# Optimization experiments

Hardware: AMD Instinct MI355X
Metric: run time of the kernel (lower is better)

Reference implementation:

```python
import jax, jax.numpy as jnp
import numpy as np

B, S, D = 2, 2048, 2048
H, DK, DV = 16, 128, 128
K_DIM = H * DK
V_DIM = H * DV
CONV_DIM = 2 * K_DIM + V_DIM
KS = 4
EPS = 1e-6


def setup_inputs() -> dict:
    key = jax.random.key(0)
    ks = jax.random.split(key, 9)
    sc = lambda k, shape, s=0.02: jax.random.normal(k, shape, jnp.float32) * s
    return {
        "hidden_states": jax.random.normal(ks[0], (B, S, D), jnp.float32),
        "attention_mask": jnp.ones((B, S), jnp.float32),
        "W_qkv": sc(ks[1], (CONV_DIM, D)),
        "conv_w": sc(ks[2], (CONV_DIM, 1, KS), 0.2),   # depthwise kernel [C,1,K]
        "conv_b": jnp.zeros((CONV_DIM,), jnp.float32),
        "W_z": sc(ks[3], (V_DIM, D)),
        "W_b": sc(ks[4], (H, D)),
        "W_a": sc(ks[5], (H, D)),
        "dt_bias": jnp.ones((H,), jnp.float32),
        "A_log": jnp.log(jax.random.uniform(ks[6], (H,), jnp.float32, 0.5, 8.0)),
        "norm_weight": jnp.zeros((DV,), jnp.float32),
        "W_out": sc(ks[7], (D, V_DIM)),
    }


def _l2norm(x):
    return x * jax.lax.rsqrt(jnp.sum(x * x, -1, keepdims=True) + 1e-6)


def _gated_delta_rule(q, k, v, g, beta):
    # q,k: [B,S,H,DK]; v: [B,S,H,DV]; g,beta: [B,S,H]
    q = _l2norm(q) * (DK ** -0.5)
    k = _l2norm(k)

    def step(state, inp):
        # state: [B,H,DK,DV]
        qt, kt, vt, gt, bt = inp
        state = state * jnp.exp(gt)[..., None, None]          # gated decay
        kv = jnp.einsum('bhk,bhkv->bhv', kt, state)           # k^T S
        delta = (vt - kv) * bt[..., None]                     # delta-rule correction
        state = state + kt[..., :, None] * delta[..., None, :]
        ot = jnp.einsum('bhk,bhkv->bhv', qt, state)
        return state, ot

    xs = tuple(jnp.moveaxis(a, 1, 0) for a in (q, k, v, g, beta))  # time-major
    state0 = jnp.zeros((B, H, DK, DV), jnp.float32)
    _, o = jax.lax.scan(step, state0, xs)
    return jnp.moveaxis(o, 0, 1)  # [B,S,H,DV]


def reference(hidden_states, attention_mask, W_qkv, conv_w, conv_b, W_z, W_b,
              W_a, dt_bias, A_log, norm_weight, W_out):
    x = hidden_states * attention_mask[:, :, None]
    mixed = jnp.einsum('bsd,cd->bsc', x, W_qkv)               # [B,S,CONV_DIM]
    # causal depthwise conv over time
    xc = jnp.moveaxis(mixed, 1, 2)                            # [B,C,S]
    xc = jax.lax.conv_general_dilated(xc, conv_w, (1,), [(KS - 1, 0)],
                                      feature_group_count=CONV_DIM)
    xc = xc + conv_b[None, :, None]
    mixed = jax.nn.silu(jnp.moveaxis(xc, 2, 1))               # [B,S,C]
    q, k, v = jnp.split(mixed, [K_DIM, 2 * K_DIM], axis=-1)
    q = q.reshape(B, S, H, DK)
    k = k.reshape(B, S, H, DK)
    v = v.reshape(B, S, H, DV)
    z = jnp.einsum('bsd,vd->bsv', x, W_z).reshape(B, S, H, DV)
    beta = jax.nn.sigmoid(jnp.einsum('bsd,hd->bsh', x, W_b))
    g = -jnp.exp(A_log) * jax.nn.softplus(jnp.einsum('bsd,hd->bsh', x, W_a) + dt_bias)
    o = _gated_delta_rule(q, k, v, g, beta)                   # [B,S,H,DV]
    # gated RMSNorm over head_v_dim
    o = o * jax.lax.rsqrt(jnp.mean(o * o, -1, keepdims=True) + EPS)
    o = o * (1.0 + norm_weight)
    o = o * jax.nn.silu(z)
    return jnp.einsum('bsv,dv->bsd', o.reshape(B, S, V_DIM), W_out)
```

## Files before the change

### kernel.cpp

```cpp
#include <hip/hip_runtime.h>
#include <hip/hip_bf16.h>
#include <math.h>

#define BB 2
#define SS 2048
#define DD 2048
#define HH 16
#define CONVC 6144
#define MM (BB*SS)

#define CH 64
#define NCH 32
#define CD_KTS 0
#define CD_TV  16384
#define CD_TP  32768
#define CD_AQ  40960
#define CD_PV  49152
#define CD_PC  49408
#define CD_STRIDE 49664

typedef __bf16 bf16_t;
typedef __bf16 bf16x8 __attribute__((ext_vector_type(8)));
typedef __bf16 bf16x4 __attribute__((ext_vector_type(4)));
typedef float  f32x4  __attribute__((ext_vector_type(4)));

#define GLOBAL_AS __attribute__((address_space(1)))
#define LDS_AS    __attribute__((address_space(3)))

#define MFMA16(a,b,c) __builtin_amdgcn_mfma_f32_16x16x32_bf16((a),(b),(c),0,0,0)

__global__ __launch_bounds__(256) void cast_all_kernel(
    const float* __restrict__ hs, const float* __restrict__ amask,
    const float* __restrict__ Wqkv, const float* __restrict__ Wz,
    const float* __restrict__ Wb, const float* __restrict__ Wa,
    const float* __restrict__ Wout,
    bf16_t* __restrict__ x_bf, bf16_t* __restrict__ wB,
    bf16_t* __restrict__ wba, bf16_t* __restrict__ woutb)
{
  const long N0 = (long)MM*DD/4;
  const long N1 = N0 + (long)CONVC*DD/4;
  const long N2 = N1 + (long)DD*DD/4;
  const long N3 = N2 + 16*DD/4;
  const long N4 = N3 + 16*DD/4;
  const long N5 = N4 + (long)DD*DD/4;
  for (long i = (long)blockIdx.x*256 + threadIdx.x; i < N5; i += (long)gridDim.x*256) {
    const float* src; bf16_t* dst; float m = 1.f;
    if (i < N0)      { long j=i;    src = hs   + j*4; dst = x_bf + j*4; m = amask[(j*4)/DD]; }
    else if (i < N1) { long j=i-N0; src = Wqkv + j*4; dst = wB + j*4; }
    else if (i < N2) { long j=i-N1; src = Wz   + j*4; dst = wB + (size_t)CONVC*DD + j*4; }
    else if (i < N3) { long j=i-N2; src = Wb   + j*4; dst = wba + j*4; }
    else if (i < N4) { long j=i-N3; src = Wa   + j*4; dst = wba + 16*DD + j*4; }
    else             { long j=i-N4; src = Wout + j*4; dst = woutb + j*4; }
    float4 v = *(const float4*)src;
    bf16x4 o4;
    o4[0]=(bf16_t)(v.x*m); o4[1]=(bf16_t)(v.y*m);
    o4[2]=(bf16_t)(v.z*m); o4[3]=(bf16_t)(v.w*m);
    *(bf16x4*)dst = o4;
  }
}

__global__ __launch_bounds__(64) void betag3_kernel(
    const bf16_t* __restrict__ xbf, const bf16_t* __restrict__ wba,
    const float* __restrict__ dtb, const float* __restrict__ Alog,
    float2* __restrict__ gb_t)
{
  const int blk = blockIdx.x;
  const int lane = threadIdx.x;
  const int fr = lane & 15, fq = lane >> 4;
  const long tok0 = (long)blk*16;

  f32x4 acc0 = {0,0,0,0}, acc1 = {0,0,0,0};
  const bf16_t* ar = xbf + (tok0 + fr)*DD + fq*8;
  const bf16_t* b0 = wba + fr*DD + fq*8;
  const bf16_t* b1 = wba + (16+fr)*DD + fq*8;
  #pragma unroll 4
  for (int ks=0; ks<64; ++ks) {
    bf16x8 a8 = *(const bf16x8*)(ar + ks*32);
    bf16x8 p8 = *(const bf16x8*)(b0 + ks*32);
    bf16x8 q8 = *(const bf16x8*)(b1 + ks*32);
    acc0 = MFMA16(a8, p8, acc0);
    acc1 = MFMA16(a8, q8, acc1);
  }
  const int h = fr;
  float eA = expf(Alog[h]);
  float db = dtb[h];
  #pragma unroll
  for (int r=0;r<4;r++) {
    long tok = tok0 + fq*4 + r;
    int b = (int)(tok >> 11), s = (int)(tok & (SS-1));
    float beta = 1.f/(1.f+expf(-acc0[r]));
    float tt2 = acc1[r] + db;
    float sp = (tt2 > 20.f) ? tt2 : log1pf(expf(tt2));
    float g  = -eA * sp;
    gb_t[((long)b*HH + h)*SS + s] = make_float2(g, beta);
  }
}

__global__ __launch_bounds__(512) void gemm_fused(
    const bf16_t* __restrict__ A, const bf16_t* __restrict__ Bm,
    bf16_t* __restrict__ Cmix, bf16_t* __restrict__ Cz, int K, int nbn)
{
  extern __shared__ char gsm[];
  const int t    = threadIdx.x;
  const int lane = t & 63;
  const int wid  = t >> 6;
  const int wm   = wid >> 2, wn = wid & 3;
  const int fr   = lane & 15, fq = lane >> 4;

  const int nwg = gridDim.x;
  const int wg  = ((int)blockIdx.x & 7)*(nwg >> 3) + ((int)blockIdx.x >> 3);
  const int grp = wg / (nbn*4);
  const int rem = wg - grp*(nbn*4);
  const long bm = grp*4 + (rem & 3);
  const long bn = rem >> 2;

  int rowS[2], colS[2];
  #pragma unroll
  for (int i=0;i<2;i++) {
    int L  = (i*512 + t)*16;
    int Ls = L ^ (((L>>9)&1)<<5);
    rowS[i] = (Ls>>10)*16 + ((Ls&1023)>>6);
    colS[i] = (Ls&63)>>1;
  }
  const bf16_t* Ab = A  + (bm*256)*(long)K;
  const bf16_t* Bb = Bm + (bn*256)*(long)K;

  f32x4 acc[8][4];
  #pragma unroll
  for (int i=0;i<8;i++)
    #pragma unroll
    for (int j=0;j<4;j++) acc[i][j] = (f32x4){0.f,0.f,0.f,0.f};

  const int aoff = fr*64 + ((fq*16) ^ ((fr&8)<<2));

  auto stage = [&](int buf, int oper, int kh, int kt) {
    const bf16_t* srcb = oper ? Bb : Ab;
    char* dst0 = gsm + oper*65536 + buf*32768 + kh*16384 + t*16;
    #pragma unroll
    for (int i=0;i<2;i++) {
      const bf16_t* src = srcb + (long)rowS[i]*K + kt*64 + kh*32 + colS[i];
      __builtin_amdgcn_global_load_lds((const GLOBAL_AS void*)src,
          (LDS_AS void*)(dst0 + i*8192), 16, 0, 0);
    }
  };

  stage(0,0,0,0); stage(0,1,0,0); stage(0,0,1,0); stage(0,1,1,0);
  asm volatile("s_waitcnt vmcnt(4)" ::: "memory");
  __builtin_amdgcn_s_barrier();

  bf16x8 bfr[4];
  int cb = 0;
  const int KT = K >> 6;
  for (int kt=0; kt<KT; ++kt) {
    const int ktn = (kt+1 < KT) ? kt+1 : kt;
    const char* abuf = gsm + cb*32768;
    const char* bbuf = gsm + 65536 + cb*32768;

    #pragma unroll
    for (int ph=0; ph<4; ph++) {
      const int kh = ph >> 1, mh = ph & 1;
      bf16x8 af[4];
      #pragma unroll
      for (int j=0;j<4;j++)
        af[j] = *(const bf16x8*)(abuf + kh*16384 + (wm*8 + mh*4 + j)*1024 + aoff);
      if (mh == 0) {
        #pragma unroll
        for (int n=0;n<4;n++)
          bfr[n] = *(const bf16x8*)(bbuf + kh*16384 + (wn*4+n)*1024 + aoff);
      }
      stage(cb^1, mh, kh, ktn);
      if (mh == 1) {
        __builtin_amdgcn_sched_barrier(0);
        asm volatile("s_waitcnt vmcnt(4)" ::: "memory");
      }
      __builtin_amdgcn_sched_barrier(0);
      __builtin_amdgcn_s_barrier();
      asm volatile("s_waitcnt lgkmcnt(0)" ::: "memory");
      __builtin_amdgcn_sched_barrier(0);
      __builtin_amdgcn_s_setprio(1);
      #pragma unroll
      for (int j=0;j<4;j++)
        #pragma unroll
        for (int n=0;n<4;n++)
          acc[mh*4+j][n] = MFMA16(af[j], bfr[n], acc[mh*4+j][n]);
      __builtin_amdgcn_s_setprio(0);
    }
    cb ^= 1;
  }
  __syncthreads();

  bf16_t* Co;
  long No, colb;
  if (bn < 24) { Co = Cmix; No = CONVC; colb = bn*256; }
  else         { Co = Cz;   No = DD;    colb = (bn-24)*256; }

  #pragma unroll
  for (int mi=0;mi<8;mi++) {
    #pragma unroll
    for (int ni=0;ni<4;ni++) {
      long row = bm*256 + wm*128 + mi*16 + fq*4;
      long col = colb + wn*64 + ni*16 + fr;
      #pragma unroll
      for (int r=0;r<4;r++)
        Co[(row+r)*No + col] = (bf16_t)acc[mi][ni][r];
    }
  }
}

template<bool OUT_BF16>
__global__ __launch_bounds__(512) void gemm256(
    const bf16_t* __restrict__ A, const bf16_t* __restrict__ Bm,
    void* __restrict__ Cp, int M, int N, int K, int nbn)
{
  extern __shared__ char gsm[];
  const int t    = threadIdx.x;
  const int lane = t & 63;
  const int wid  = t >> 6;
  const int wm   = wid >> 2, wn = wid & 3;
  const int fr   = lane & 15, fq = lane >> 4;

  const int nwg = gridDim.x;
  const int wg  = ((int)blockIdx.x & 7)*(nwg >> 3) + ((int)blockIdx.x >> 3);
  const int grp = wg / (nbn*4);
  const int rem = wg - grp*(nbn*4);
  const long bm = grp*4 + (rem & 3);
  const long bn = rem >> 2;

  int rowS[2], colS[2];
  #pragma unroll
  for (int i=0;i<2;i++) {
    int L  = (i*512 + t)*16;
    int Ls = L ^ (((L>>9)&1)<<5);
    rowS[i] = (Ls>>10)*16 + ((Ls&1023)>>6);
    colS[i] = (Ls&63)>>1;
  }
  const bf16_t* Ab = A  + (bm*256)*(long)K;
  const bf16_t* Bb = Bm + (bn*128)*(long)K;

  f32x4 acc[8][2];
  #pragma unroll
  for (int i=0;i<8;i++) { acc[i][0] = (f32x4){0,0,0,0}; acc[i][1] = (f32x4){0,0,0,0}; }

  const int aoff = fr*64 + ((fq*16) ^ ((fr&8)<<2));

  auto stageA = [&](int buf, int kh, int kt) {
    char* dst0 = gsm + buf*32768 + kh*16384 + t*16;
    #pragma unroll
    for (int i=0;i<2;i++) {
      const bf16_t* src = Ab + (long)rowS[i]*K + kt*64 + kh*32 + colS[i];
      __builtin_amdgcn_global_load_lds((const GLOBAL_AS void*)src,
          (LDS_AS void*)(dst0 + i*8192), 16, 0, 0);
    }
  };
  auto stageB = [&](int buf, int kh, int kt) {
    char* dst = gsm + 65536 + buf*16384 + kh*8192 + t*16;
    const bf16_t* src = Bb + (long)rowS[0]*K + kt*64 + kh*32 + colS[0];
    __builtin_amdgcn_global_load_lds((const GLOBAL_AS void*)src,
        (LDS_AS void*)dst, 16, 0, 0);
  };

  stageA(0,0,0); stageB(0,0,0); stageA(0,1,0); stageB(0,1,0);
  asm volatile("s_waitcnt vmcnt(3)" ::: "memory");
  __builtin_amdgcn_s_barrier();

  int cb = 0;
  const int KT = K >> 6;
  for (int kt=0; kt<KT; ++kt) {
    const int ktn = (kt+1 < KT) ? kt+1 : kt;
    const char* abuf = gsm + cb*32768;
    const char* bbuf = gsm + 65536 + cb*16384;

    #pragma unroll
    for (int kh=0; kh<2; kh++) {
      bf16x8 af[8], bfr[2];
      #pragma unroll
      for (int j=0;j<8;j++)
        af[j] = *(const bf16x8*)(abuf + kh*16384 + (wm*8+j)*1024 + aoff);
      #pragma unroll
      for (int n=0;n<2;n++)
        bfr[n] = *(const bf16x8*)(bbuf + kh*8192 + (wn*2+n)*1024 + aoff);
      stageA(cb^1, kh, ktn);
      stageB(cb^1, kh, ktn);
      asm volatile("s_waitcnt vmcnt(3)" ::: "memory");
      __builtin_amdgcn_sched_barrier(0);
      __builtin_amdgcn_s_barrier();
      asm volatile("s_waitcnt lgkmcnt(0)" ::: "memory");
      __builtin_amdgcn_sched_barrier(0);
      __builtin_amdgcn_s_setprio(1);
      #pragma unroll
      for (int j=0;j<8;j++)
        #pragma unroll
        for (int n=0;n<2;n++)
          acc[j][n] = MFMA16(af[j], bfr[n], acc[j][n]);
      __builtin_amdgcn_s_setprio(0);
    }
    cb ^= 1;
  }
  __syncthreads();

  #pragma unroll
  for (int mi=0;mi<8;mi++) {
    #pragma unroll
    for (int ni=0;ni<2;ni++) {
      long row = bm*256 + wm*128 + mi*16 + fq*4;
      long col = bn*128 + wn*32 + ni*16 + fr;
      #pragma unroll
      for (int r=0;r<4;r++) {
        float v = acc[mi][ni][r];
        if (OUT_BF16) ((bf16_t*)Cp)[(row+r)*(long)N + col] = (bf16_t)v;
        else          ((float*)Cp)[(row+r)*(long)N + col] = v;
      }
    }
  }
}

__global__ __launch_bounds__(256) void conv_norm_kernel(
    const bf16_t* __restrict__ mixed, const float* __restrict__ cw,
    const float* __restrict__ cb, bf16_t* __restrict__ q_t,
    bf16_t* __restrict__ k_t, bf16_t* __restrict__ v_t)
{
  __shared__ bf16_t lx[35*392];
  __shared__ float4 lcw[384];
  __shared__ float  lcb[384];
  const int blk = blockIdx.x;
  const int st = blk & 63;
  const int h  = (blk >> 6) & 15;
  const int b  = blk >> 10;
  const int t  = threadIdx.x;
  const int s0 = st*32;

  for (int i = t; i < 384; i += 256) {
    int seg = i >> 7, d = i & 127;
    int gch = seg*2048 + h*128 + d;
    lcw[i] = ((const float4*)cw)[gch];
    lcb[i] = cb[gch];
  }
  for (int idx = t; idx < 1680; idx += 256) {
    int chunk = idx >> 4, e = idx & 15;
    int row = chunk / 3, seg = chunk - row*3;
    int s2 = s0 - 3 + row;
    bf16x8 v8;
    if (s2 >= 0) {
      v8 = *(const bf16x8*)(mixed + ((long)b*SS + s2)*CONVC + seg*2048 + h*128 + e*8);
    } else {
      #pragma unroll
      for (int j=0;j<8;j++) v8[j] = (bf16_t)0.f;
    }
    *(bf16x8*)&lx[row*392 + seg*128 + e*8] = v8;
  }
  __syncthreads();

  const int s_local = t >> 3, dg = t & 7;
  const int s  = s0 + s_local;
  const int d0 = dg*16;
  const long obase = ((long)(b*HH + h)*SS + s)*128 + d0;

  float scl_q = 0.f, scl_k = 0.f;

  #pragma unroll
  for (int seg=0; seg<3; ++seg) {
    bf16x8 xr[4][2];
    #pragma unroll
    for (int tp=0; tp<4; ++tp) {
      const bf16_t* p = &lx[(s_local + tp)*392 + seg*128 + d0];
      xr[tp][0] = *(const bf16x8*)p;
      xr[tp][1] = *(const bf16x8*)(p + 8);
    }
    float a[16];
    #pragma unroll
    for (int half=0; half<2; ++half) {
      #pragma unroll
      for (int j=0;j<8;j++) {
        int ch = seg*128 + d0 + half*8 + j;
        float4 wj = lcw[ch];
        float v = lcb[ch]
                + (float)xr[0][half][j]*wj.x + (float)xr[1][half][j]*wj.y
                + (float)xr[2][half][j]*wj.z + (float)xr[3][half][j]*wj.w;
        a[half*8+j] = v * (1.f/(1.f+expf(-v)));
      }
    }
    if (seg < 2) {
      float ss = 0.f;
      #pragma unroll
      for (int j=0;j<16;j++) ss += a[j]*a[j];
      ss += __shfl_xor(ss, 1);
      ss += __shfl_xor(ss, 2);
      ss += __shfl_xor(ss, 4);
      float scl = rsqrtf(ss + 1e-6f);
      if (seg == 0) scl_q = scl * 0.08838834764831845f;
      else          scl_k = scl;
    }
    {
      bf16_t* outp = (seg==0) ? (q_t + obase) : (seg==1) ? (k_t + obase) : (v_t + obase);
      float scl = (seg==0) ? scl_q : (seg==1) ? scl_k : 1.f;
      bf16x8 o0, o1;
      #pragma unroll
      for (int j=0;j<8;j++) { o0[j] = (bf16_t)(a[j]*scl); o1[j] = (bf16_t)(a[8+j]*scl); }
      *(bf16x8*)outp = o0;
      *(bf16x8*)(outp + 8) = o1;
    }
  }
}

__global__ __launch_bounds__(256) void chunkA_kernel(
    const bf16_t* __restrict__ q_t, const bf16_t* __restrict__ k_t,
    const bf16_t* __restrict__ v_t, const float2* __restrict__ gb_t,
    char* __restrict__ cdata)
{
  extern __shared__ char smem[];
  bf16_t* lK  = (bf16_t*)(smem);
  bf16_t* lQV = (bf16_t*)(smem + 17408);
  float*  lLf = (float*)(smem + 35840);
  float*  lXf = (float*)(smem + 52480);
  float*  gcv = (float*)(smem + 69120);
  float*  pvv = (float*)(smem + 69376);
  float*  bvv = (float*)(smem + 69632);
  float*  evv = (float*)(smem + 69888);
  float*  lP  = (float*)(smem + 70144);

  const int cd = blockIdx.x;
  const int bh = cd >> 5, c = cd & 31;
  const int t = threadIdx.x;
  const int lane = t & 63, w = t >> 6;
  const int fr = lane & 15, fq = lane >> 4;

  const bf16_t* kg = k_t + ((long)bh*SS + c*CH)*128;
  const bf16_t* qg = q_t + ((long)bh*SS + c*CH)*128;
  const bf16_t* vg = v_t + ((long)bh*SS + c*CH)*128;
  char* cdp = cdata + (long)cd*CD_STRIDE;

  #pragma unroll
  for (int ib=0; ib<4; ib++) {
    int e0 = (t + 256*ib)*8;
    int r = e0 >> 7, cc = e0 & 127;
    *(bf16x8*)&lK[r*136+cc]  = *(const bf16x8*)(kg + e0);
    *(bf16x8*)&lQV[r*136+cc] = *(const bf16x8*)(qg + e0);
  }
  if (t < 64) {
    float2 gb = gb_t[(long)bh*SS + c*CH + t];
    gcv[t] = gb.x;
    bvv[t] = gb.y;
  }
  __syncthreads();
  if (t < 64) {
    float g = gcv[t];
    #pragma unroll
    for (int off=1; off<64; off<<=1) {
      float n = __shfl_up(g, off);
      if (lane >= off) g += n;
    }
    gcv[t] = g;
  }
  __syncthreads();
  if (t < 64) {
    pvv[t] = expf(gcv[t]);
    evv[t] = expf(gcv[63] - gcv[t]);
  }

  {
    f32x4 accG[4], accQ[4];
    #pragma unroll
    for (int tn=0;tn<4;tn++){ accG[tn]=(f32x4){0,0,0,0}; accQ[tn]=(f32x4){0,0,0,0}; }
    #pragma unroll
    for (int ks=0;ks<4;ks++) {
      bf16x8 aK = *(const bf16x8*)&lK[(w*16+fr)*136 + fq*8 + ks*32];
      bf16x8 aQ = *(const bf16x8*)&lQV[(w*16+fr)*136 + fq*8 + ks*32];
      #pragma unroll
      for (int tn=0;tn<4;tn++) {
        bf16x8 bK = *(const bf16x8*)&lK[(tn*16+fr)*136 + fq*8 + ks*32];
        accG[tn] = MFMA16(aK, bK, accG[tn]);
        accQ[tn] = MFMA16(aQ, bK, accQ[tn]);
      }
    }
    bf16_t* aqg = (bf16_t*)(cdp + CD_AQ);
    #pragma unroll
    for (int tn=0;tn<4;tn++) {
      #pragma unroll
      for (int r=0;r<4;r++) {
        int tt = w*16 + fq*4 + r;
        int ii = tn*16 + fr;
        float er = expf(gcv[tt] - gcv[ii]);
        lLf[tt*65 + ii] = (ii < tt) ? bvv[tt]*er*accG[tn][r] : 0.f;
        aqg[tt*64 + ii] = (bf16_t)((ii <= tt) ? er*accQ[tn][r] : 0.f);
      }
    }
  }

  {
    const int a = w;
    float* Ub = lXf + (a*16)*65 + a*16;
    const float* Lb = lLf + (a*16)*65 + a*16;
    if (lane < 16) Ub[lane] = (lane == 0) ? 1.f : 0.f;
    for (int bb = a+1; bb < 4; bb++)
      for (int e = lane; e < 256; e += 64)
        lXf[(a*16 + (e>>4))*65 + bb*16 + (e&15)] = 0.f;
    if (lane < 16) {
      const int cc = lane;
      for (int i=1; i<16; i++) {
        float s = 0.f;
        for (int j=0; j<i; j++) s += Lb[i*65+j] * Ub[j*65+cc];
        Ub[i*65+cc] = ((i==cc)?1.f:0.f) - s;
      }
    }
  }
  __syncthreads();

  bf16_t* lVT = lQV;
  {
    const int m = t & 15;
    #pragma unroll
    for (int ib=0; ib<4; ib++) {
      int e0 = (t + 256*ib)*8;
      int r = e0 >> 7, cc = e0 & 127;
      bf16x8 v8 = *(const bf16x8*)(vg + e0);
      #pragma unroll
      for (int e=0;e<8;e++) {
        int ee = (e + m) & 7;
        lVT[(cc+ee)*72 + r] = v8[ee];
      }
    }
  }

  {
    const int i = t >> 4, j = t & 15;
    #pragma unroll
    for (int bb=0; bb<3; bb++) {
      float s = 0.f;
      const float* Mrow = lLf + ((bb+1)*16 + i)*65 + bb*16;
      const float* Ucol = lXf + (bb*16)*65 + bb*16 + j;
      #pragma unroll
      for (int k=0;k<16;k++) s += Mrow[k] * Ucol[k*65];
      lP[bb*272 + i*17 + j] = s;
    }
  }
  __syncthreads();
  {
    const int i = t >> 4, j = t & 15;
    #pragma unroll
    for (int bb=0; bb<3; bb++) {
      float s = 0.f;
      const float* Urow = lXf + ((bb+1)*16 + i)*65 + (bb+1)*16;
      const float* Pcol = lP + bb*272 + j;
      #pragma unroll
      for (int k=0;k<16;k++) s += Urow[k] * Pcol[k*17];
      lXf[((bb+1)*16 + i)*65 + bb*16 + j] = -s;
    }
  }
  __syncthreads();
  {
    const int i = t >> 4, j = t & 15;
    #pragma unroll
    for (int bb=0; bb<2; bb++) {
      float s = 0.f;
      const float* M0 = lLf + ((bb+2)*16 + i)*65 + bb*16;
      const float* U0 = lXf + (bb*16)*65 + bb*16 + j;
      const float* M1 = lLf + ((bb+2)*16 + i)*65 + (bb+1)*16;
      const float* T1 = lXf + ((bb+1)*16)*65 + bb*16 + j;
      #pragma unroll
      for (int k=0;k<16;k++) s += M0[k]*U0[k*65] + M1[k]*T1[k*65];
      lP[bb*272 + i*17 + j] = s;
    }
  }
  __syncthreads();
  {
    const int i = t >> 4, j = t & 15;
    #pragma unroll
    for (int bb=0; bb<2; bb++) {
      float s = 0.f;
      const float* Urow = lXf + ((bb+2)*16 + i)*65 + (bb+2)*16;
      const float* Pcol = lP + bb*272 + j;
      #pragma unroll
      for (int k=0;k<16;k++) s += Urow[k] * Pcol[k*17];
      lXf[((bb+2)*16 + i)*65 + bb*16 + j] = -s;
    }
  }
  __syncthreads();
  {
    const int i = t >> 4, j = t & 15;
    float s = 0.f;
    const float* M0 = lLf + (48 + i)*65 + 0;
    const float* U0 = lXf + 0*65 + j;
    const float* M1 = lLf + (48 + i)*65 + 16;
    const float* T1 = lXf + 16*65 + j;
    const float* M2 = lLf + (48 + i)*65 + 32;
    const float* T2 = lXf + 32*65 + j;
    #pragma unroll
    for (int k=0;k<16;k++) s += M0[k]*U0[k*65] + M1[k]*T1[k*65] + M2[k]*T2[k*65];
    lP[i*17 + j] = s;
  }
  __syncthreads();
  {
    const int i = t >> 4, j = t & 15;
    float s = 0.f;
    const float* Urow = lXf + (48 + i)*65 + 48;
    const float* Pcol = lP + j;
    #pragma unroll
    for (int k=0;k<16;k++) s += Urow[k] * Pcol[k*17];
    lXf[(48 + i)*65 + j] = -s;
  }
  __syncthreads();

  bf16_t* lXb = (bf16_t*)lLf;
  {
    bf16_t* tpg = (bf16_t*)(cdp + CD_TP);
    #pragma unroll
    for (int ib=0; ib<16; ib++) {
      int idx = t + ib*256; int r = idx>>6, cc = idx&63;
      float xv = lXf[r*65+cc] * bvv[cc];
      tpg[r*64+cc] = (bf16_t)(xv * pvv[cc]);
      lXb[r*72+cc] = (bf16_t)xv;
    }
  }
  __syncthreads();

  {
    f32x4 acc[8];
    #pragma unroll
    for (int tn=0;tn<8;tn++) acc[tn]=(f32x4){0,0,0,0};
    #pragma unroll
    for (int ks=0;ks<2;ks++) {
      bf16x8 aX = *(const bf16x8*)&lXb[(w*16+fr)*72 + fq*8 + ks*32];
      #pragma unroll
      for (int tn=0;tn<8;tn++) {
        bf16x8 bV = *(const bf16x8*)&lVT[(tn*16+fr)*72 + fq*8 + ks*32];
        acc[tn] = MFMA16(aX, bV, acc[tn]);
      }
    }
    bf16_t* tvg = (bf16_t*)(cdp + CD_TV);
    #pragma unroll
    for (int tn=0;tn<8;tn++)
      #pragma unroll
      for (int r=0;r<4;r++) {
        int tt = w*16 + fq*4 + r, dv = tn*16 + fr;
        tvg[tt*128 + dv] = (bf16_t)acc[tn][r];
      }
  }

  {
    bf16_t* ktg = (bf16_t*)(cdp + CD_KTS);
    int dk = t >> 1, c0 = (t & 1)*32;
    bf16_t tmp[32];
    #pragma unroll
    for (int i2=0;i2<32;i2++) {
      int i = c0 + i2;
      tmp[i2] = (bf16_t)((float)lK[i*136 + dk] * evv[i]);
    }
    #pragma unroll
    for (int s8=0;s8<4;s8++)
      *(bf16x8*)&ktg[dk*64 + c0 + s8*8] = *(bf16x8*)&tmp[s8*8];
  }
  if (t < 64) ((float*)(cdp + CD_PV))[t] = pvv[t];
  if (t == 0) *((float*)(cdp + CD_PC)) = expf(gcv[63]);
}

__global__ __launch_bounds__(256) void chunkS_kernel(
    const bf16_t* __restrict__ q_t, const bf16_t* __restrict__ k_t,
    const char* __restrict__ cdata, bf16_t* __restrict__ gD,
    bf16_t* __restrict__ gXq)
{
  extern __shared__ char smem[];
  float*  lS  = (float*)(smem);
  bf16_t* lSb = (bf16_t*)(smem + 8320);
  bf16_t* lK  = (bf16_t*)(smem + 12672);
  bf16_t* lQ  = (bf16_t*)(smem + 30080);
  bf16_t* lTp = (bf16_t*)(smem + 47488);
  bf16_t* lKT = (bf16_t*)(smem + 56704);
  bf16_t* lXT = (bf16_t*)(smem + 75136);
  bf16_t* lDT = (bf16_t*)(smem + 77952);

  const int bid = blockIdx.x;
  const int lb  = (bid & 7)*32 + (bid >> 3);
  const int bh = lb >> 3, sp = lb & 7;
  const int dv0 = sp*16;
  const int t = threadIdx.x, lane = t & 63, w = t >> 6;
  const int fr = lane & 15, fq = lane >> 4;

  #pragma unroll
  for (int ib=0; ib<8; ib++) {
    int idx = t + ib*256; int r = idx>>7, cc = idx&127;
    lS[r*129+cc] = 0.f;
    lSb[r*136+cc] = (bf16_t)0.f;
  }

  const bf16_t* kg = k_t + (long)bh*SS*128;
  const bf16_t* qg = q_t + (long)bh*SS*128;

  bf16x8 kr0,kr1,kr2,kr3, qr0,qr1,qr2,qr3, kt0,kt1,kt2,kt3, tp0,tp1;

#define STAGE_LOAD(CSRC)                                                       \
  {                                                                            \
    const char* cdl = cdata + (long)(bh*NCH + (CSRC))*CD_STRIDE;               \
    const bf16_t* kl = kg + (long)(CSRC)*CH*128;                               \
    const bf16_t* ql = qg + (long)(CSRC)*CH*128;                               \
    const bf16_t* ktl = (const bf16_t*)(cdl + CD_KTS);                         \
    const bf16_t* tpl = (const bf16_t*)(cdl + CD_TP);                          \
    int e0 = t*8, e1 = (t+256)*8, e2 = (t+512)*8, e3 = (t+768)*8;              \
    kr0 = *(const bf16x8*)(kl + e0); kr1 = *(const bf16x8*)(kl + e1);          \
    kr2 = *(const bf16x8*)(kl + e2); kr3 = *(const bf16x8*)(kl + e3);          \
    qr0 = *(const bf16x8*)(ql + e0); qr1 = *(const bf16x8*)(ql + e1);          \
    qr2 = *(const bf16x8*)(ql + e2); qr3 = *(const bf16x8*)(ql + e3);          \
    kt0 = *(const bf16x8*)(ktl + e0); kt1 = *(const bf16x8*)(ktl + e1);        \
    kt2 = *(const bf16x8*)(ktl + e2); kt3 = *(const bf16x8*)(ktl + e3);        \
    tp0 = *(const bf16x8*)(tpl + e0); tp1 = *(const bf16x8*)(tpl + e1);        \
  }

#define STAGE_WRITE()                                                          \
  {                                                                            \
    int e0 = t*8, e1 = (t+256)*8, e2 = (t+512)*8, e3 = (t+768)*8;              \
    *(bf16x8*)&lK[(e0>>7)*136 + (e0&127)] = kr0;                               \
    *(bf16x8*)&lK[(e1>>7)*136 + (e1&127)] = kr1;                               \
    *(bf16x8*)&lK[(e2>>7)*136 + (e2&127)] = kr2;                               \
    *(bf16x8*)&lK[(e3>>7)*136 + (e3&127)] = kr3;                               \
    *(bf16x8*)&lQ[(e0>>7)*136 + (e0&127)] = qr0;                               \
    *(bf16x8*)&lQ[(e1>>7)*136 + (e1&127)] = qr1;                               \
    *(bf16x8*)&lQ[(e2>>7)*136 + (e2&127)] = qr2;                               \
    *(bf16x8*)&lQ[(e3>>7)*136 + (e3&127)] = qr3;                               \
    *(bf16x8*)&lKT[(e0>>6)*72 + (e0&63)] = kt0;                                \
    *(bf16x8*)&lKT[(e1>>6)*72 + (e1&63)] = kt1;                                \
    *(bf16x8*)&lKT[(e2>>6)*72 + (e2&63)] = kt2;                                \
    *(bf16x8*)&lKT[(e3>>6)*72 + (e3&63)] = kt3;                                \
    *(bf16x8*)&lTp[(e0>>6)*72 + (e0&63)] = tp0;                                \
    *(bf16x8*)&lTp[(e1>>6)*72 + (e1&63)] = tp1;                                \
  }

  STAGE_LOAD(0);
  STAGE_WRITE();
  __syncthreads();

  for (int c=0; c<NCH; c++) {
    const int cd = bh*NCH + c;
    const char* cdp = cdata + (long)cd*CD_STRIDE;

    float tvq0, tvq1, tvq2, tvq3, pc;
    {
      const bf16_t* tvp = (const bf16_t*)(cdp + CD_TV);
      tvq0 = (float)tvp[(w*16+fq*4+0)*128 + dv0 + fr];
      tvq1 = (float)tvp[(w*16+fq*4+1)*128 + dv0 + fr];
      tvq2 = (float)tvp[(w*16+fq*4+2)*128 + dv0 + fr];
      tvq3 = (float)tvp[(w*16+fq*4+3)*128 + dv0 + fr];
      pc = *(const float*)(cdp + CD_PC);
    }
    const int cn = (c+1 < NCH) ? c+1 : c;
    STAGE_LOAD(cn);

    f32x4 aX = {0,0,0,0}, aXq = {0,0,0,0};
    #pragma unroll
    for (int ks=0; ks<4; ks++) {
      bf16x8 bS = *(const bf16x8*)&lSb[fr*136 + fq*8 + ks*32];
      bf16x8 aK = *(const bf16x8*)&lK[(w*16+fr)*136 + fq*8 + ks*32];
      bf16x8 aQ = *(const bf16x8*)&lQ[(w*16+fr)*136 + fq*8 + ks*32];
      aX  = MFMA16(aK, bS, aX);
      aXq = MFMA16(aQ, bS, aXq);
    }
    #pragma unroll
    for (int r=0;r<4;r++)
      lXT[fr*88 + (w*16+fq*4+r)] = (bf16_t)aX[r];
    __syncthreads();

    {
      f32x4 aD = {0,0,0,0};
      #pragma unroll
      for (int ks=0; ks<2; ks++) {
        bf16x8 aT = *(const bf16x8*)&lTp[(w*16+fr)*72 + fq*8 + ks*32];
        bf16x8 bX = *(const bf16x8*)&lXT[fr*88 + fq*8 + ks*32];
        aD = MFMA16(aT, bX, aD);
      }
      lDT[fr*88 + (w*16+fq*4+0)] = (bf16_t)(tvq0 - aD[0]);
      lDT[fr*88 + (w*16+fq*4+1)] = (bf16_t)(tvq1 - aD[1]);
      lDT[fr*88 + (w*16+fq*4+2)] = (bf16_t)(tvq2 - aD[2]);
      lDT[fr*88 + (w*16+fq*4+3)] = (bf16_t)(tvq3 - aD[3]);
    }
    #pragma unroll
    for (int ib=0; ib<8; ib++) {
      int idx = t + ib*256; int r = idx>>7, cc = idx&127;
      lS[r*129+cc] *= pc;
    }
    __syncthreads();

    {
      f32x4 aS0 = {0,0,0,0}, aS1 = {0,0,0,0};
      #pragma unroll
      for (int ks=0; ks<2; ks++) {
        bf16x8 aDd = *(const bf16x8*)&lDT[fr*88 + fq*8 + ks*32];
        bf16x8 bK0 = *(const bf16x8*)&lKT[(w*32+fr)*72 + fq*8 + ks*32];
        bf16x8 bK1 = *(const bf16x8*)&lKT[(w*32+16+fr)*72 + fq*8 + ks*32];
        aS0 = MFMA16(aDd, bK0, aS0);
        aS1 = MFMA16(aDd, bK1, aS1);
      }
      #pragma unroll
      for (int r=0;r<4;r++) {
        lS[(fq*4+r)*129 + w*32 + fr]      += aS0[r];
        lS[(fq*4+r)*129 + w*32 + 16 + fr] += aS1[r];
      }
    }
    #pragma unroll
    for (int r=0;r<4;r++)
      gXq[((long)cd*CH + w*16+fq*4+r)*128 + dv0 + fr] = (bf16_t)aXq[r];
    {
      int dvl = t >> 4, off = (t & 15)*4;
      *(bf16x4*)(gD + ((long)cd*128 + dv0 + dvl)*64 + off) =
          *(const bf16x4*)&lDT[dvl*88 + off];
    }
    __syncthreads();

    STAGE_WRITE();
    #pragma unroll
    for (int ib=0; ib<8; ib++) {
      int idx = t + ib*256; int r = idx>>7, cc = idx&127;
      lSb[r*136+cc] = (bf16_t)lS[r*129+cc];
    }
    __syncthreads();
  }
#undef STAGE_LOAD
#undef STAGE_WRITE
}

__global__ __launch_bounds__(256) void chunkO_kernel(
    const char* __restrict__ cdata, const bf16_t* __restrict__ gD,
    const bf16_t* __restrict__ gXq, const bf16_t* __restrict__ zfull,
    const float* __restrict__ nw, bf16_t* __restrict__ og)
{
  const int cd = blockIdx.x;
  const int bh = cd >> 5, c = cd & 31;
  const int b = bh >> 4, h = bh & 15;
  const int t = threadIdx.x, lane = t & 63, w = t >> 6;
  const int fr = lane & 15, fq = lane >> 4;

  const char* cdp = cdata + (long)cd*CD_STRIDE;
  const bf16_t* aqp = (const bf16_t*)(cdp + CD_AQ);
  const bf16_t* dp  = gD + (long)cd*128*64;
  const float*  pvp = (const float*)(cdp + CD_PV);

  f32x4 acc[8];
  #pragma unroll
  for (int tn=0;tn<8;tn++) acc[tn]=(f32x4){0,0,0,0};
  #pragma unroll
  for (int ks=0;ks<2;ks++) {
    bf16x8 aA = *(const bf16x8*)(aqp + (w*16+fr)*64 + fq*8 + ks*32);
    #pragma unroll
    for (int tn=0;tn<8;tn++) {
      bf16x8 bD = *(const bf16x8*)(dp + (tn*16+fr)*64 + fq*8 + ks*32);
      acc[tn] = MFMA16(aA, bD, acc[tn]);
    }
  }

  float ov[8][4];
  float ssum[4] = {0.f, 0.f, 0.f, 0.f};
  #pragma unroll
  for (int tn=0;tn<8;tn++)
    #pragma unroll
    for (int r=0;r<4;r++) {
      int tt = w*16+fq*4+r, dv = tn*16+fr;
      float v = pvp[tt]*(float)gXq[((long)cd*CH + tt)*128 + dv] + acc[tn][r];
      ov[tn][r] = v;
      ssum[r] += v*v;
    }
  #pragma unroll
  for (int r=0;r<4;r++) {
    ssum[r] += __shfl_xor(ssum[r], 1);
    ssum[r] += __shfl_xor(ssum[r], 2);
    ssum[r] += __shfl_xor(ssum[r], 4);
    ssum[r] += __shfl_xor(ssum[r], 8);
  }
  float rr[4];
  #pragma unroll
  for (int r=0;r<4;r++) rr[r] = rsqrtf(ssum[r]*(1.f/128.f) + 1e-6f);

  #pragma unroll
  for (int tn=0;tn<8;tn++) {
    #pragma unroll
    for (int r=0;r<4;r++) {
      int tt = w*16+fq*4+r, dv = tn*16+fr;
      long tok = (long)b*SS + c*CH + tt;
      float zn = (float)zfull[tok*DD + h*128 + dv];
      float val = ov[tn][r] * rr[r] * (1.f + nw[dv]) * (zn * (1.f/(1.f+expf(-zn))));
      og[(tok*HH + h)*128 + dv] = (bf16_t)val;
    }
  }
}

extern "C" void kernel_launch(void* const* d_in, const int* in_sizes, int n_in,
                              void* d_out, int out_size, void* d_ws, size_t ws_size,
                              hipStream_t stream)
{
  const float* hs    = (const float*)d_in[0];
  const float* amask = (const float*)d_in[1];
  const float* Wqkv  = (const float*)d_in[2];
  const float* convw = (const float*)d_in[3];
  const float* convb = (const float*)d_in[4];
  const float* Wz    = (const float*)d_in[5];
  const float* Wb    = (const float*)d_in[6];
  const float* Wa    = (const float*)d_in[7];
  const float* dtb   = (const float*)d_in[8];
  const float* Alog  = (const float*)d_in[9];
  const float* nw    = (const float*)d_in[10];
  const float* Wout  = (const float*)d_in[11];

  const size_t MB = 1024*1024;
  char* p = (char*)d_ws;
  auto alloc = [&](size_t bytes) { char* r = p; p += (bytes + 255) & ~(size_t)255; return r; };
  bf16_t* x_bf   = (bf16_t*)alloc(16*MB);
  char*   bigreg = alloc(84*MB);
  bf16_t* wba    = (bf16_t*)alloc(256*1024);
  bf16_t* woutb  = (bf16_t*)alloc(8*MB);
  bf16_t* zbuf   = (bf16_t*)alloc(16*MB);
  bf16_t* q_t    = (bf16_t*)alloc(16*MB);
  bf16_t* k_t    = (bf16_t*)alloc(16*MB);
  bf16_t* v_t    = (bf16_t*)alloc(16*MB);
  float2* gb_t   = (float2*)alloc((size_t)BB*HH*SS*8);
  size_t need = (size_t)(p - (char*)d_ws);
  if (ws_size < need) return;

  bf16_t* wB      = (bf16_t*)bigreg;
  bf16_t* mixed   = (bf16_t*)(bigreg + 34*MB);
  char*   cdata   = bigreg;
  bf16_t* gD      = x_bf;
  bf16_t* gXq     = v_t;
  bf16_t* og      = q_t;

  cast_all_kernel<<<2048, 256, 0, stream>>>(hs, amask, Wqkv, Wz, Wb, Wa, Wout,
                                            x_bf, wB, wba, woutb);

  betag3_kernel<<<MM/16, 64, 0, stream>>>(x_bf, wba, dtb, Alog, gb_t);

  gemm_fused<<<512, 512, 131072, stream>>>(x_bf, wB, mixed, zbuf, DD, 32);

  conv_norm_kernel<<<BB*HH*(SS/32), 256, 0, stream>>>(mixed, convw, convb, q_t, k_t, v_t);

  chunkA_kernel<<<BB*HH*NCH, 256, 73408, stream>>>(q_t, k_t, v_t, gb_t, cdata);
  chunkS_kernel<<<BB*HH*8, 256, 80768, stream>>>(q_t, k_t, cdata, gD, gXq);
  chunkO_kernel<<<BB*HH*NCH, 256, 0, stream>>>(cdata, gD, gXq, zbuf, nw, og);

  gemm256<false><<<256, 512, 98304, stream>>>(og, woutb, d_out, MM, DD, DD, 16);
}
```

Measured before the change: 380.3 us.

## Fuse intra-chunk output into chunkS and split out RMSNorm gating kernel

Moves the per-chunk output computation (Aq times delta plus decayed inter-chunk term) into the sequential chunkS kernel using its on-chip delta tile, so it no longer writes gD and gXq to global memory. A new lightweight per-(token,head) kernel then applies the gated RMSNorm, because each chunkS block only holds 16 value columns and cannot reduce over all 128. This removes intermediate global traffic and the chunkO kernel, but adds MFMA and LDS work (plus about 9KB more shared memory) to the latency-critical sequential kernel, and adds a small-block norm launch with 65536 blocks.

```diff
diff --git a/kernel.cpp b/kernel.cpp
--- a/kernel.cpp
+++ b/kernel.cpp
@@ -655,8 +655,7 @@
 
 __global__ __launch_bounds__(256) void chunkS_kernel(
     const bf16_t* __restrict__ q_t, const bf16_t* __restrict__ k_t,
-    const char* __restrict__ cdata, bf16_t* __restrict__ gD,
-    bf16_t* __restrict__ gXq)
+    const char* __restrict__ cdata, bf16_t* __restrict__ obuf)
 {
   extern __shared__ char smem[];
   float*  lS  = (float*)(smem);
@@ -667,11 +666,13 @@
   bf16_t* lKT = (bf16_t*)(smem + 56704);
   bf16_t* lXT = (bf16_t*)(smem + 75136);
   bf16_t* lDT = (bf16_t*)(smem + 77952);
+  bf16_t* lAq = (bf16_t*)(smem + 80768);
 
   const int bid = blockIdx.x;
   const int lb  = (bid & 7)*32 + (bid >> 3);
   const int bh = lb >> 3, sp = lb & 7;
   const int dv0 = sp*16;
+  const int b = bh >> 4, h = bh & 15;
   const int t = threadIdx.x, lane = t & 63, w = t >> 6;
   const int fr = lane & 15, fq = lane >> 4;
 
@@ -685,7 +686,7 @@
   const bf16_t* kg = k_t + (long)bh*SS*128;
   const bf16_t* qg = q_t + (long)bh*SS*128;
 
-  bf16x8 kr0,kr1,kr2,kr3, qr0,qr1,qr2,qr3, kt0,kt1,kt2,kt3, tp0,tp1;
+  bf16x8 kr0,kr1,kr2,kr3, qr0,qr1,qr2,qr3, kt0,kt1,kt2,kt3, tp0,tp1, aq0,aq1;
 
 #define STAGE_LOAD(CSRC)                                                       \
   {                                                                            \
@@ -694,6 +695,7 @@
     const bf16_t* ql = qg + (long)(CSRC)*CH*128;                               \
     const bf16_t* ktl = (const bf16_t*)(cdl + CD_KTS);                         \
     const bf16_t* tpl = (const bf16_t*)(cdl + CD_TP);                          \
+    const bf16_t* aql = (const bf16_t*)(cdl + CD_AQ);                          \
     int e0 = t*8, e1 = (t+256)*8, e2 = (t+512)*8, e3 = (t+768)*8;              \
     kr0 = *(const bf16x8*)(kl + e0); kr1 = *(const bf16x8*)(kl + e1);          \
     kr2 = *(const bf16x8*)(kl + e2); kr3 = *(const bf16x8*)(kl + e3);          \
@@ -702,6 +704,7 @@
     kt0 = *(const bf16x8*)(ktl + e0); kt1 = *(const bf16x8*)(ktl + e1);        \
     kt2 = *(const bf16x8*)(ktl + e2); kt3 = *(const bf16x8*)(ktl + e3);        \
     tp0 = *(const bf16x8*)(tpl + e0); tp1 = *(const bf16x8*)(tpl + e1);        \
+    aq0 = *(const bf16x8*)(aql + e0); aq1 = *(const bf16x8*)(aql + e1);        \
   }
 
 #define STAGE_WRITE()                                                          \
@@ -721,6 +724,8 @@
     *(bf16x8*)&lKT[(e3>>6)*72 + (e3&63)] = kt3;                                \
     *(bf16x8*)&lTp[(e0>>6)*72 + (e0&63)] = tp0;                                \
     *(bf16x8*)&lTp[(e1>>6)*72 + (e1&63)] = tp1;                                \
+    *(bf16x8*)&lAq[(e0>>6)*72 + (e0&63)] = aq0;                                \
+    *(bf16x8*)&lAq[(e1>>6)*72 + (e1&63)] = aq1;                                \
   }
 
   STAGE_LOAD(0);
@@ -732,12 +737,16 @@
     const char* cdp = cdata + (long)cd*CD_STRIDE;
 
     float tvq0, tvq1, tvq2, tvq3, pc;
+    float pvq[4];
     {
       const bf16_t* tvp = (const bf16_t*)(cdp + CD_TV);
+      const float* pvp = (const float*)(cdp + CD_PV);
       tvq0 = (float)tvp[(w*16+fq*4+0)*128 + dv0 + fr];
       tvq1 = (float)tvp[(w*16+fq*4+1)*128 + dv0 + fr];
       tvq2 = (float)tvp[(w*16+fq*4+2)*128 + dv0 + fr];
       tvq3 = (float)tvp[(w*16+fq*4+3)*128 + dv0 + fr];
+      #pragma unroll
+      for (int r=0;r<4;r++) pvq[r] = pvp[w*16+fq*4+r];
       pc = *(const float*)(cdp + CD_PC);
     }
     const int cn = (c+1 < NCH) ? c+1 : c;
@@ -778,28 +787,30 @@
     __syncthreads();
 
     {
-      f32x4 aS0 = {0,0,0,0}, aS1 = {0,0,0,0};
+      f32x4 aS0 = {0,0,0,0}, aS1 = {0,0,0,0}, aO = {0,0,0,0};
       #pragma unroll
       for (int ks=0; ks<2; ks++) {
         bf16x8 aDd = *(const bf16x8*)&lDT[fr*88 + fq*8 + ks*32];
         bf16x8 bK0 = *(const bf16x8*)&lKT[(w*32+fr)*72 + fq*8 + ks*32];
         bf16x8 bK1 = *(const bf16x8*)&lKT[(w*32+16+fr)*72 + fq*8 + ks*32];
+        bf16x8 aA  = *(const bf16x8*)&lAq[(w*16+fr)*72 + fq*8 + ks*32];
+        bf16x8 bD  = *(const bf16x8*)&lDT[fr*88 + fq*8 + ks*32];
         aS0 = MFMA16(aDd, bK0, aS0);
         aS1 = MFMA16(aDd, bK1, aS1);
+        aO  = MFMA16(aA,  bD,  aO);
       }
       #pragma unroll
       for (int r=0;r<4;r++) {
         lS[(fq*4+r)*129 + w*32 + fr]      += aS0[r];
         lS[(fq*4+r)*129 + w*32 + 16 + fr] += aS1[r];
       }
-    }
-    #pragma unroll
-    for (int r=0;r<4;r++)
-      gXq[((long)cd*CH + w*16+fq*4+r)*128 + dv0 + fr] = (bf16_t)aXq[r];
-    {
-      int dvl = t >> 4, off = (t & 15)*4;
-      *(bf16x4*)(gD + ((long)cd*128 + dv0 + dvl)*64 + off) =
-          *(const bf16x4*)&lDT[dvl*88 + off];
+      #pragma unroll
+      for (int r=0;r<4;r++) {
+        int tt = w*16+fq*4+r;
+        long tok = (long)b*SS + c*CH + tt;
+        float ov = pvq[r]*aXq[r] + aO[r];
+        obuf[(tok*HH + h)*128 + dv0 + fr] = (bf16_t)ov;
+      }
     }
     __syncthreads();
 
@@ -815,68 +826,25 @@
 #undef STAGE_WRITE
 }
 
-__global__ __launch_bounds__(256) void chunkO_kernel(
-    const char* __restrict__ cdata, const bf16_t* __restrict__ gD,
-    const bf16_t* __restrict__ gXq, const bf16_t* __restrict__ zfull,
+__global__ __launch_bounds__(128) void norm_gate_kernel(
+    const bf16_t* __restrict__ o, const bf16_t* __restrict__ zfull,
     const float* __restrict__ nw, bf16_t* __restrict__ og)
 {
-  const int cd = blockIdx.x;
-  const int bh = cd >> 5, c = cd & 31;
-  const int b = bh >> 4, h = bh & 15;
-  const int t = threadIdx.x, lane = t & 63, w = t >> 6;
-  const int fr = lane & 15, fq = lane >> 4;
-
-  const char* cdp = cdata + (long)cd*CD_STRIDE;
-  const bf16_t* aqp = (const bf16_t*)(cdp + CD_AQ);
-  const bf16_t* dp  = gD + (long)cd*128*64;
-  const float*  pvp = (const float*)(cdp + CD_PV);
-
-  f32x4 acc[8];
-  #pragma unroll
-  for (int tn=0;tn<8;tn++) acc[tn]=(f32x4){0,0,0,0};
-  #pragma unroll
-  for (int ks=0;ks<2;ks++) {
-    bf16x8 aA = *(const bf16x8*)(aqp + (w*16+fr)*64 + fq*8 + ks*32);
-    #pragma unroll
-    for (int tn=0;tn<8;tn++) {
-      bf16x8 bD = *(const bf16x8*)(dp + (tn*16+fr)*64 + fq*8 + ks*32);
-      acc[tn] = MFMA16(aA, bD, acc[tn]);
-    }
-  }
-
-  float ov[8][4];
-  float ssum[4] = {0.f, 0.f, 0.f, 0.f};
-  #pragma unroll
-  for (int tn=0;tn<8;tn++)
-    #pragma unroll
-    for (int r=0;r<4;r++) {
-      int tt = w*16+fq*4+r, dv = tn*16+fr;
-      float v = pvp[tt]*(float)gXq[((long)cd*CH + tt)*128 + dv] + acc[tn][r];
-      ov[tn][r] = v;
-      ssum[r] += v*v;
-    }
-  #pragma unroll
-  for (int r=0;r<4;r++) {
-    ssum[r] += __shfl_xor(ssum[r], 1);
-    ssum[r] += __shfl_xor(ssum[r], 2);
-    ssum[r] += __shfl_xor(ssum[r], 4);
-    ssum[r] += __shfl_xor(ssum[r], 8);
-  }
-  float rr[4];
-  #pragma unroll
-  for (int r=0;r<4;r++) rr[r] = rsqrtf(ssum[r]*(1.f/128.f) + 1e-6f);
-
-  #pragma unroll
-  for (int tn=0;tn<8;tn++) {
-    #pragma unroll
-    for (int r=0;r<4;r++) {
-      int tt = w*16+fq*4+r, dv = tn*16+fr;
-      long tok = (long)b*SS + c*CH + tt;
-      float zn = (float)zfull[tok*DD + h*128 + dv];
-      float val = ov[tn][r] * rr[r] * (1.f + nw[dv]) * (zn * (1.f/(1.f+expf(-zn))));
-      og[(tok*HH + h)*128 + dv] = (bf16_t)val;
-    }
-  }
+  const long row = blockIdx.x;
+  const long tok = row >> 4;
+  const int h = row & 15;
+  const int d = threadIdx.x;
+  float x = (float)o[row*128 + d];
+  float ss = x*x;
+  #pragma unroll
+  for (int off=32; off>=1; off>>=1) ss += __shfl_xor(ss, off);
+  __shared__ float red[2];
+  if ((d & 63) == 0) red[d>>6] = ss;
+  __syncthreads();
+  float mean = (red[0] + red[1]) * (1.f/128.f);
+  float zn = (float)zfull[tok*DD + h*128 + d];
+  float val = x * rsqrtf(mean + 1e-6f) * (1.f + nw[d]) * (zn * (1.f/(1.f+expf(-zn))));
+  og[row*128 + d] = (bf16_t)val;
 }
 
 extern "C" void kernel_launch(void* const* d_in, const int* in_sizes, int n_in,
@@ -914,8 +882,7 @@
   bf16_t* wB      = (bf16_t*)bigreg;
   bf16_t* mixed   = (bf16_t*)(bigreg + 34*MB);
   char*   cdata   = bigreg;
-  bf16_t* gD      = x_bf;
-  bf16_t* gXq     = v_t;
+  bf16_t* obuf    = v_t;
   bf16_t* og      = q_t;
 
   cast_all_kernel<<<2048, 256, 0, stream>>>(hs, amask, Wqkv, Wz, Wb, Wa, Wout,
@@ -928,8 +895,9 @@
   conv_norm_kernel<<<BB*HH*(SS/32), 256, 0, stream>>>(mixed, convw, convb, q_t, k_t, v_t);
 
   chunkA_kernel<<<BB*HH*NCH, 256, 73408, stream>>>(q_t, k_t, v_t, gb_t, cdata);
-  chunkS_kernel<<<BB*HH*8, 256, 80768, stream>>>(q_t, k_t, cdata, gD, gXq);
-  chunkO_kernel<<<BB*HH*NCH, 256, 0, stream>>>(cdata, gD, gXq, zbuf, nw, og);
+  chunkS_kernel<<<BB*HH*8, 256, 89984, stream>>>(q_t, k_t, cdata, obuf);
+
+  norm_gate_kernel<<<MM*HH, 128, 0, stream>>>(obuf, zbuf, nw, og);
 
   gemm256<false><<<256, 512, 98304, stream>>>(og, woutb, d_out, MM, DD, DD, 16);
 }
```

Measured after the change: 381.5 us. About the same (+0.3%).
